# Kernel tuning notes

Hardware: AMD Instinct MI355X
Metric: run time of the kernel (lower is better)

Reference implementation:

```python
import jax, jax.numpy as jnp
import numpy as np

DIM = 384
HEADS = 6
HEAD_DIM = DIM // HEADS
HIDDEN = 4 * DIM
EPS = 1e-5


def layer_norm(x, w, b):
    m = jnp.mean(x, axis=-1, keepdims=True)
    v = jnp.mean((x - m) ** 2, axis=-1, keepdims=True)
    return (x - m) * jax.lax.rsqrt(v + EPS) * w + b


def setup_inputs() -> dict:
    key = jax.random.key(0)
    ks = jax.random.split(key, 8)
    B, N = 2, 4096
    s_in = 1.0 / np.sqrt(DIM)
    s_h = 1.0 / np.sqrt(HIDDEN)
    return {
        "x": jax.random.normal(ks[0], (B, N, DIM), dtype=jnp.float32),
        "qkv_w": jax.random.normal(ks[1], (3 * DIM, DIM), dtype=jnp.float32) * s_in,
        "proj_w": jax.random.normal(ks[2], (DIM, DIM), dtype=jnp.float32) * s_in,
        "proj_b": jnp.zeros((DIM,), dtype=jnp.float32),
        "ln1_w": jnp.ones((DIM,), dtype=jnp.float32),
        "ln1_b": jnp.zeros((DIM,), dtype=jnp.float32),
        "ln2_w": jnp.ones((DIM,), dtype=jnp.float32),
        "ln2_b": jnp.zeros((DIM,), dtype=jnp.float32),
        "fc1_w": jax.random.normal(ks[3], (HIDDEN, DIM), dtype=jnp.float32) * s_in,
        "fc1_b": jnp.zeros((HIDDEN,), dtype=jnp.float32),
        "fc2_w": jax.random.normal(ks[4], (DIM, HIDDEN), dtype=jnp.float32) * s_h,
        "fc2_b": jnp.zeros((DIM,), dtype=jnp.float32),
    }


def reference(x, qkv_w, proj_w, proj_b, ln1_w, ln1_b, ln2_w, ln2_b,
              fc1_w, fc1_b, fc2_w, fc2_b):
    B, N, C = x.shape
    scale = HEAD_DIM ** (-0.5)

    # pre-norm attention
    y = layer_norm(x, ln1_w, ln1_b)
    qkv = (y @ qkv_w.T).reshape(B, N, 3, HEADS, HEAD_DIM)
    qkv = jnp.transpose(qkv, (2, 0, 3, 1, 4))  # [3, B, H, N, D]
    q, k, v = qkv[0], qkv[1], qkv[2]
    attn = jnp.einsum("bhnd,bhmd->bhnm", q, k) * scale  # [B,H,N,N]
    attn = jax.nn.softmax(attn, axis=-1)
    y = jnp.einsum("bhnm,bhmd->bhnd", attn, v)
    y = jnp.transpose(y, (0, 2, 1, 3)).reshape(B, N, C)
    y = y @ proj_w.T + proj_b

    # residual + LN2 + MLP (faithful to source: output = 2 * mlp(ln2(x + y)))
    x = x + y
    x = layer_norm(x, ln2_w, ln2_b)
    h = jax.nn.gelu(x @ fc1_w.T + fc1_b, approximate=False)
    x = h @ fc2_w.T + fc2_b
    x = x + x
    return x
```

## Files before the change

### kernel.cpp

```cpp
#include <hip/hip_runtime.h>
#include <hip/hip_bf16.h>

#define DIM 384
#define HEADS 6
#define HD 64
#define HIDDEN 1536
#define SEQ 4096
#define BATCH 2
#define NTOK (BATCH*SEQ)
#define QKVN (3*DIM)

typedef __attribute__((ext_vector_type(4))) float f32x4;
typedef __attribute__((ext_vector_type(16))) float f32x16;
typedef __attribute__((ext_vector_type(8))) short s16x8;
typedef __attribute__((ext_vector_type(4))) unsigned int u32x4;

__device__ __forceinline__ ushort f2bf(float f) {
    union { float f; unsigned u; } v; v.f = f;
    unsigned r = v.u + 0x7FFF + ((v.u >> 16) & 1);
    return (ushort)(r >> 16);
}
__device__ __forceinline__ float bf2f(ushort b) {
    union { unsigned u; float f; } v; v.u = ((unsigned)b) << 16;
    return v.f;
}
__device__ __forceinline__ unsigned cvtpk(float lo, float hi) {
    unsigned r;
    asm("v_cvt_pk_bf16_f32 %0, %1, %2" : "=v"(r) : "v"(lo), "v"(hi));
    return r;
}
__device__ __forceinline__ void pl32swap(unsigned& a, unsigned& b) {
    asm volatile("v_permlane32_swap_b32 %0, %1" : "+v"(a), "+v"(b));
}
__device__ __forceinline__ void g2l(const ushort* g, ushort* s) {
    __builtin_amdgcn_global_load_lds((const __attribute__((address_space(1))) void*)g,
                                     (__attribute__((address_space(3))) void*)s, 16, 0, 0);
}

__global__ void cvt4_kernel(const float4* __restrict__ s0, ushort* __restrict__ d0, int n0,
                            const float4* __restrict__ s1, ushort* __restrict__ d1, int n1,
                            const float4* __restrict__ s2, ushort* __restrict__ d2, int n2,
                            const float4* __restrict__ s3, ushort* __restrict__ d3, int n3) {
    int i = blockIdx.x * 256 + threadIdx.x;
    const float4* s; ushort* d; int k = i;
    if (i < n0) { s = s0; d = d0; }
    else { k -= n0; if (k < n1) { s = s1; d = d1; }
        else { k -= n1; if (k < n2) { s = s2; d = d2; }
            else { k -= n2; if (k >= n3) return; s = s3; d = d3; } } }
    float4 v = s[k];
    ushort4 o; o.x = f2bf(v.x); o.y = f2bf(v.y); o.z = f2bf(v.z); o.w = f2bf(v.w);
    *(ushort4*)(d + (size_t)k * 4) = o;
}

__global__ __launch_bounds__(256) void ln_kernel(const float* __restrict__ x,
        const float* __restrict__ w, const float* __restrict__ b,
        ushort* __restrict__ y) {
    int l = threadIdx.x & 63;
    int row = blockIdx.x * 4 + (threadIdx.x >> 6);
    const float* xr = x + (size_t)row * DIM;
    float v[6], s = 0.f, s2 = 0.f;
#pragma unroll
    for (int i = 0; i < 6; ++i) { v[i] = xr[l + 64*i]; s += v[i]; s2 += v[i]*v[i]; }
#pragma unroll
    for (int d = 1; d < 64; d <<= 1) { s += __shfl_xor(s, d); s2 += __shfl_xor(s2, d); }
    float mean = s * (1.f/DIM);
    float var  = s2 * (1.f/DIM) - mean*mean;
    float rstd = rsqrtf(var + 1e-5f);
    ushort* yr = y + (size_t)row * DIM;
#pragma unroll
    for (int i = 0; i < 6; ++i) {
        int c = l + 64*i;
        yr[c] = f2bf((v[i]-mean)*rstd*w[c] + b[c]);
    }
}

template<int EPI, int BN>
__global__ __launch_bounds__(256, 4) void gemm_kernel(
        const ushort* __restrict__ A, const ushort* __restrict__ W,
        const float* __restrict__ bias, const float* __restrict__ resid,
        void* __restrict__ Cout, int M, int N, int K) {
    __shared__ __align__(16) ushort lds_a[64*64];
    __shared__ __align__(16) ushort lds_w[BN*64];
    const int t = threadIdx.x, l = t & 63, wid = t >> 6;
    const int lo = l & 15, lg = l >> 4;
    const int m0 = blockIdx.x * 64, n0 = blockIdx.y * BN;
    constexpr int NI = BN / 32;
    constexpr int WW = BN / 32;
    const int wm = (wid & 1) * 32, wn = (wid >> 1) * (BN / 2);
    f32x4 acc[2][NI] = {};

    const int srow8 = l >> 3;
    const int schunk = (l & 7) ^ srow8;
    const ushort* gA[2];
    ushort* lA[2];
#pragma unroll
    for (int w = 0; w < 2; ++w) {
        gA[w] = A + (size_t)(m0 + wid*16 + w*8 + srow8) * K + schunk*8;
        lA[w] = &lds_a[(wid*16 + w*8)*64];
    }
    const ushort* gW[WW];
    ushort* lW[WW];
#pragma unroll
    for (int w = 0; w < WW; ++w) {
        gW[w] = W + (size_t)(n0 + wid*(8*WW) + w*8 + srow8) * K + schunk*8;
        lW[w] = &lds_w[(wid*(8*WW) + w*8)*64];
    }

    const int lo7 = lo & 7;
    for (int k0 = 0; k0 < K; k0 += 64) {
        if (k0) __syncthreads();
#pragma unroll
        for (int w = 0; w < 2; ++w)  g2l(gA[w] + k0, lA[w]);
#pragma unroll
        for (int w = 0; w < WW; ++w) g2l(gW[w] + k0, lW[w]);
        __syncthreads();
#pragma unroll
        for (int kk = 0; kk < 2; ++kk) {
            const int ch = ((kk*4 + lg) ^ lo7) * 8;
            s16x8 af[2], bfr[NI];
#pragma unroll
            for (int mi = 0; mi < 2; ++mi)
                af[mi] = *(const s16x8*)&lds_a[(wm + mi*16 + lo)*64 + ch];
#pragma unroll
            for (int ni = 0; ni < NI; ++ni)
                bfr[ni] = *(const s16x8*)&lds_w[(wn + ni*16 + lo)*64 + ch];
#pragma unroll
            for (int mi = 0; mi < 2; ++mi)
#pragma unroll
                for (int ni = 0; ni < NI; ++ni)
                    acc[mi][ni] = __builtin_amdgcn_mfma_f32_16x16x32_bf16(af[mi], bfr[ni], acc[mi][ni], 0,0,0);
        }
    }

#pragma unroll
    for (int mi = 0; mi < 2; ++mi)
#pragma unroll
    for (int ni = 0; ni < NI; ++ni)
#pragma unroll
    for (int r = 0; r < 4; ++r) {
        int row = m0 + wm + mi*16 + lg*4 + r;
        int col = n0 + wn + ni*16 + lo;
        float c = acc[mi][ni][r];
        size_t idx = (size_t)row * N + col;
        if (EPI == 0) {
            ((ushort*)Cout)[idx] = f2bf(c);
        } else if (EPI == 1) {
            ((float*)Cout)[idx] = c + bias[col] + resid[idx];
        } else if (EPI == 2) {
            c += bias[col];
            ((ushort*)Cout)[idx] = f2bf(0.5f * c * (1.f + erff(c * 0.70710678118f)));
        } else {
            ((float*)Cout)[idx] = 2.f * (c + bias[col]);
        }
    }
}

#define PV_STEP(S, MM, CB) do {                                                   \
    unsigned w0 = cvtpk(S[8*MM+0], S[8*MM+1]);                                    \
    unsigned w1 = cvtpk(S[8*MM+2], S[8*MM+3]);                                    \
    unsigned w2 = cvtpk(S[8*MM+4], S[8*MM+5]);                                    \
    unsigned w3 = cvtpk(S[8*MM+6], S[8*MM+7]);                                    \
    pl32swap(w0, w2); pl32swap(w1, w3);                                           \
    u32x4 fw = {w0, w1, w2, w3};                                                  \
    s16x8 pa = __builtin_bit_cast(s16x8, fw);                                     \
    int colb = ((CB) + G*8) ^ swz0;                                               \
    s16x8 vb0 = *(const s16x8*)&lds_v[half][q31][colb];                           \
    s16x8 vb1 = *(const s16x8*)&lds_v[half][32 + q31][colb ^ 32];                 \
    o0 = __builtin_amdgcn_mfma_f32_32x32x16_bf16(pa, vb0, o0, 0,0,0);             \
    o1 = __builtin_amdgcn_mfma_f32_32x32x16_bf16(pa, vb1, o1, 0,0,0);             \
    ol = __builtin_amdgcn_mfma_f32_32x32x16_bf16(pa, vones, ol, 0,0,0);           \
} while (0)

__global__ __launch_bounds__(256, 3) void attn_kernel(const ushort* __restrict__ qkv,
                                                      ushort* __restrict__ out) {
    __shared__ __align__(16) ushort lds_k[2][64][72];
    __shared__ __align__(16) ushort lds_v[2][64][72];
    const int t = threadIdx.x, l = t & 63, wid = t >> 6;
    const int G = l >> 5, q31 = l & 31, half = wid >> 1;
    const int b = blockIdx.y / HEADS, h = blockIdx.y % HEADS;
    const ushort* base = qkv + (size_t)b * SEQ * QKVN + h * HD;
    const int q0 = blockIdx.x * 64 + (wid & 1) * 32;

    const float QSC = 0.1803368801111137f;
    s16x8 qf[4];
#pragma unroll
    for (int dc = 0; dc < 4; ++dc) {
        s16x8 qv = *(const s16x8*)(base + (size_t)(q0 + q31) * QKVN + dc*16 + G*8);
#pragma unroll
        for (int j = 0; j < 8; ++j)
            qv[j] = (short)f2bf(bf2f((ushort)qv[j]) * QSC);
        qf[dc] = qv;
    }
    s16x8 vones;
#pragma unroll
    for (int j = 0; j < 8; ++j) vones[j] = (short)0x3F80;

    f32x16 o0 = {}, o1 = {}, ol = {};

    const int u = t & 127, sa = u >> 3, sc = u & 7;
    const ushort* kbase = base + DIM;
    const ushort* vbase = base + 2*DIM;
    const int key0base = half * (SEQ/2);
    const int swz0 = ((q31 >> 3) & 3) << 3;

    s16x8 kreg[4], vreg[4];
#pragma unroll
    for (int p = 0; p < 4; ++p) {
        kreg[p] = *(const s16x8*)(kbase + (size_t)(key0base + p*16 + sa) * QKVN + sc*8);
        vreg[p] = *(const s16x8*)(vbase + (size_t)(key0base + p*16 + sa) * QKVN + sc*8);
    }

    for (int it = 0; it < 32; ++it) {
        const int key0 = key0base + it*64;
        __syncthreads();
#pragma unroll
        for (int p = 0; p < 4; ++p) {
            *(s16x8*)&lds_k[half][p*16 + sa][sc*8] = kreg[p];
            const int colp = (p*16 + sa) ^ ((sc & 3) << 3) ^ ((sc >> 2) << 5);
#pragma unroll
            for (int j = 0; j < 8; ++j)
                lds_v[half][sc*8 + j][colp] = (ushort)vreg[p][j];
        }
        __syncthreads();
        if (it < 31) {
#pragma unroll
            for (int p = 0; p < 4; ++p) {
                kreg[p] = *(const s16x8*)(kbase + (size_t)(key0 + 64 + p*16 + sa) * QKVN + sc*8);
                vreg[p] = *(const s16x8*)(vbase + (size_t)(key0 + 64 + p*16 + sa) * QKVN + sc*8);
            }
        }

        f32x16 st0 = {}, st1 = {};
        __builtin_amdgcn_s_setprio(1);
#pragma unroll
        for (int dc = 0; dc < 4; ++dc) {
            s16x8 kf0 = *(const s16x8*)&lds_k[half][q31][dc*16 + G*8];
            s16x8 kf1 = *(const s16x8*)&lds_k[half][32 + q31][dc*16 + G*8];
            st0 = __builtin_amdgcn_mfma_f32_32x32x16_bf16(kf0, qf[dc], st0, 0,0,0);
            st1 = __builtin_amdgcn_mfma_f32_32x32x16_bf16(kf1, qf[dc], st1, 0,0,0);
        }
        __builtin_amdgcn_s_setprio(0);

#pragma unroll
        for (int r = 0; r < 16; ++r) {
            st0[r] = exp2f(st0[r]);
            st1[r] = exp2f(st1[r]);
        }

        __builtin_amdgcn_s_setprio(1);
        PV_STEP(st0, 0, 0);
        PV_STEP(st0, 1, 16);
        PV_STEP(st1, 0, 32);
        PV_STEP(st1, 1, 48);
        __builtin_amdgcn_s_setprio(0);
    }

    __syncthreads();
    float* mb = (float*)&lds_k[0][0][0];
    float* ml = (float*)&lds_v[0][0][0];
    if (half == 1) {
#pragma unroll
        for (int r = 0; r < 16; ++r) {
            mb[((wid&1)*2 + 0)*1024 + r*64 + l] = o0[r];
            mb[((wid&1)*2 + 1)*1024 + r*64 + l] = o1[r];
            ml[(wid&1)*1024 + r*64 + l] = ol[r];
        }
    }
    __syncthreads();
    if (half == 0) {
        ushort* ob = out + (size_t)b * SEQ * DIM + h * HD;
#pragma unroll
        for (int r = 0; r < 16; ++r) {
            float invr = 1.0f / (ol[r] + ml[(wid&1)*1024 + r*64 + l]);
            float v0 = (o0[r] + mb[((wid&1)*2 + 0)*1024 + r*64 + l]) * invr;
            float v1 = (o1[r] + mb[((wid&1)*2 + 1)*1024 + r*64 + l]) * invr;
            int qr = (r & 3) + 8*(r >> 2) + 4*G;
            int row = q0 + qr;
            ob[(size_t)row * DIM + q31]      = f2bf(v0);
            ob[(size_t)row * DIM + 32 + q31] = f2bf(v1);
        }
    }
}

extern "C" void kernel_launch(void* const* d_in, const int* in_sizes, int n_in,
                              void* d_out, int out_size, void* d_ws, size_t ws_size,
                              hipStream_t stream) {
    const float* x      = (const float*)d_in[0];
    const float* qkv_w  = (const float*)d_in[1];
    const float* proj_w = (const float*)d_in[2];
    const float* proj_b = (const float*)d_in[3];
    const float* ln1_w  = (const float*)d_in[4];
    const float* ln1_b  = (const float*)d_in[5];
    const float* ln2_w  = (const float*)d_in[6];
    const float* ln2_b  = (const float*)d_in[7];
    const float* fc1_w  = (const float*)d_in[8];
    const float* fc1_b  = (const float*)d_in[9];
    const float* fc2_w  = (const float*)d_in[10];
    const float* fc2_b  = (const float*)d_in[11];
    float* outp = (float*)d_out;

    char* ws = (char*)d_ws;
    size_t off = 0;
    auto alloc = [&](size_t bytes) {
        off = (off + 255) & ~(size_t)255;
        void* p = ws + off;
        off += bytes;
        return p;
    };
    ushort* wq   = (ushort*)alloc((size_t)QKVN * DIM * 2);
    ushort* wp   = (ushort*)alloc((size_t)DIM * DIM * 2);
    ushort* w1   = (ushort*)alloc((size_t)HIDDEN * DIM * 2);
    ushort* w2   = (ushort*)alloc((size_t)DIM * HIDDEN * 2);
    ushort* y1   = (ushort*)alloc((size_t)NTOK * DIM * 2);
    ushort* qkvb = (ushort*)alloc((size_t)NTOK * QKVN * 2);
    ushort* ao   = (ushort*)alloc((size_t)NTOK * DIM * 2);
    float*  res  = (float*) alloc((size_t)NTOK * DIM * 4);
    ushort* y2   = (ushort*)alloc((size_t)NTOK * DIM * 2);
    ushort* hb   = (ushort*)alloc((size_t)NTOK * HIDDEN * 2);

    const int n0 = QKVN*DIM/4, n1 = DIM*DIM/4, n2 = HIDDEN*DIM/4, n3 = DIM*HIDDEN/4;
    cvt4_kernel<<<(n0+n1+n2+n3 + 255)/256, 256, 0, stream>>>(
        (const float4*)qkv_w, wq, n0, (const float4*)proj_w, wp, n1,
        (const float4*)fc1_w, w1, n2, (const float4*)fc2_w, w2, n3);

    ln_kernel<<<NTOK/4, 256, 0, stream>>>(x, ln1_w, ln1_b, y1);
    gemm_kernel<0,128><<<dim3(NTOK/64, QKVN/128), 256, 0, stream>>>(y1, wq, nullptr, nullptr, qkvb, NTOK, QKVN, DIM);
    attn_kernel<<<dim3(SEQ/64, BATCH*HEADS), 256, 0, stream>>>(qkvb, ao);
    gemm_kernel<1,64><<<dim3(NTOK/64, DIM/64), 256, 0, stream>>>(ao, wp, proj_b, x, res, NTOK, DIM, DIM);
    ln_kernel<<<NTOK/4, 256, 0, stream>>>(res, ln2_w, ln2_b, y2);
    gemm_kernel<2,128><<<dim3(NTOK/64, HIDDEN/128), 256, 0, stream>>>(y2, w1, fc1_b, nullptr, hb, NTOK, HIDDEN, DIM);
    gemm_kernel<3,64><<<dim3(NTOK/64, DIM/64), 256, 0, stream>>>(hb, w2, fc2_b, nullptr, outp, NTOK, DIM, HIDDEN);
}
```

Measured before the change: 248.3 us.

## Double-buffer GEMM LDS tiles with async global-to-LDS prefetch

```diff
diff --git a/kernel.cpp b/kernel.cpp
--- a/kernel.cpp
+++ b/kernel.cpp
@@ -35,6 +35,11 @@
 __device__ __forceinline__ void g2l(const ushort* g, ushort* s) {
     __builtin_amdgcn_global_load_lds((const __attribute__((address_space(1))) void*)g,
                                      (__attribute__((address_space(3))) void*)s, 16, 0, 0);
+}
+__device__ __forceinline__ void blockbar() {
+    asm volatile("" ::: "memory");
+    __builtin_amdgcn_s_barrier();
+    asm volatile("" ::: "memory");
 }
 
 __global__ void cvt4_kernel(const float4* __restrict__ s0, ushort* __restrict__ d0, int n0,
@@ -75,12 +80,12 @@
 }
 
 template<int EPI, int BN>
-__global__ __launch_bounds__(256, 4) void gemm_kernel(
+__global__ __launch_bounds__(256, (BN == 128 ? 3 : 4)) void gemm_kernel(
         const ushort* __restrict__ A, const ushort* __restrict__ W,
         const float* __restrict__ bias, const float* __restrict__ resid,
         void* __restrict__ Cout, int M, int N, int K) {
-    __shared__ __align__(16) ushort lds_a[64*64];
-    __shared__ __align__(16) ushort lds_w[BN*64];
+    __shared__ __align__(16) ushort lds_a[2][64*64];
+    __shared__ __align__(16) ushort lds_w[2][BN*64];
     const int t = threadIdx.x, l = t & 63, wid = t >> 6;
     const int lo = l & 15, lg = l >> 4;
     const int m0 = blockIdx.x * 64, n0 = blockIdx.y * BN;
@@ -92,45 +97,65 @@
     const int srow8 = l >> 3;
     const int schunk = (l & 7) ^ srow8;
     const ushort* gA[2];
-    ushort* lA[2];
-#pragma unroll
-    for (int w = 0; w < 2; ++w) {
+#pragma unroll
+    for (int w = 0; w < 2; ++w)
         gA[w] = A + (size_t)(m0 + wid*16 + w*8 + srow8) * K + schunk*8;
-        lA[w] = &lds_a[(wid*16 + w*8)*64];
-    }
     const ushort* gW[WW];
-    ushort* lW[WW];
-#pragma unroll
-    for (int w = 0; w < WW; ++w) {
+#pragma unroll
+    for (int w = 0; w < WW; ++w)
         gW[w] = W + (size_t)(n0 + wid*(8*WW) + w*8 + srow8) * K + schunk*8;
-        lW[w] = &lds_w[(wid*(8*WW) + w*8)*64];
-    }
+
+#define STAGE(BUF, K0) do {                                                    \
+    _Pragma("unroll")                                                          \
+    for (int w = 0; w < 2; ++w)  g2l(gA[w] + (K0), &lds_a[BUF][(wid*16 + w*8)*64]); \
+    _Pragma("unroll")                                                          \
+    for (int w = 0; w < WW; ++w) g2l(gW[w] + (K0), &lds_w[BUF][(wid*(8*WW) + w*8)*64]); \
+} while (0)
+
+#define WAITC do {                                                             \
+    if constexpr (BN == 128) asm volatile("s_waitcnt vmcnt(6)" ::: "memory");  \
+    else                     asm volatile("s_waitcnt vmcnt(4)" ::: "memory");  \
+} while (0)
+#define WAIT0 asm volatile("s_waitcnt vmcnt(0)" ::: "memory")
 
     const int lo7 = lo & 7;
-    for (int k0 = 0; k0 < K; k0 += 64) {
-        if (k0) __syncthreads();
-#pragma unroll
-        for (int w = 0; w < 2; ++w)  g2l(gA[w] + k0, lA[w]);
-#pragma unroll
-        for (int w = 0; w < WW; ++w) g2l(gW[w] + k0, lW[w]);
-        __syncthreads();
-#pragma unroll
-        for (int kk = 0; kk < 2; ++kk) {
-            const int ch = ((kk*4 + lg) ^ lo7) * 8;
-            s16x8 af[2], bfr[NI];
-#pragma unroll
-            for (int mi = 0; mi < 2; ++mi)
-                af[mi] = *(const s16x8*)&lds_a[(wm + mi*16 + lo)*64 + ch];
-#pragma unroll
-            for (int ni = 0; ni < NI; ++ni)
-                bfr[ni] = *(const s16x8*)&lds_w[(wn + ni*16 + lo)*64 + ch];
-#pragma unroll
-            for (int mi = 0; mi < 2; ++mi)
-#pragma unroll
-                for (int ni = 0; ni < NI; ++ni)
-                    acc[mi][ni] = __builtin_amdgcn_mfma_f32_16x16x32_bf16(af[mi], bfr[ni], acc[mi][ni], 0,0,0);
-        }
-    }
+#define COMPUTE(BUF) do {                                                      \
+    _Pragma("unroll")                                                          \
+    for (int kk = 0; kk < 2; ++kk) {                                           \
+        const int ch = ((kk*4 + lg) ^ lo7) * 8;                                \
+        s16x8 af[2], bfr[NI];                                                  \
+        _Pragma("unroll")                                                      \
+        for (int mi = 0; mi < 2; ++mi)                                         \
+            af[mi] = *(const s16x8*)&lds_a[BUF][(wm + mi*16 + lo)*64 + ch];    \
+        _Pragma("unroll")                                                      \
+        for (int ni = 0; ni < NI; ++ni)                                        \
+            bfr[ni] = *(const s16x8*)&lds_w[BUF][(wn + ni*16 + lo)*64 + ch];   \
+        _Pragma("unroll")                                                      \
+        for (int mi = 0; mi < 2; ++mi)                                         \
+            _Pragma("unroll")                                                  \
+            for (int ni = 0; ni < NI; ++ni)                                    \
+                acc[mi][ni] = __builtin_amdgcn_mfma_f32_16x16x32_bf16(af[mi], bfr[ni], acc[mi][ni], 0,0,0); \
+    }                                                                          \
+} while (0)
+
+    STAGE(0, 0);
+    int k0 = 0, remaining = K / 64;
+    while (true) {
+        if (remaining > 1) { STAGE(1, k0 + 64); WAITC; } else WAIT0;
+        blockbar();
+        COMPUTE(0);
+        blockbar();
+        k0 += 64; if (--remaining == 0) break;
+        if (remaining > 1) { STAGE(0, k0 + 64); WAITC; } else WAIT0;
+        blockbar();
+        COMPUTE(1);
+        blockbar();
+        k0 += 64; if (--remaining == 0) break;
+    }
+#undef STAGE
+#undef WAITC
+#undef WAIT0
+#undef COMPUTE
 
 #pragma unroll
     for (int mi = 0; mi < 2; ++mi)
```

New measurement: 248.7 us. No clear change (+0.1%).
